# Kernel tuning notes

Measured on AMD Instinct MI355X. Metric: run time of the kernel, lower is better.

## Reference

```python
import jax, jax.numpy as jnp
import numpy as np

B, T, C, H = 4, 2048, 1024, 16
HD = C // H  # head_dim = 64

def setup_inputs() -> dict:
    key = jax.random.key(0)
    k1, k2, k3 = jax.random.split(key, 3)
    x = jax.random.normal(k1, (B, T, C), dtype=jnp.float32)
    w_qkv = jax.random.normal(k2, (C, 3 * C), dtype=jnp.float32) * (C ** -0.5)
    b_qkv = jnp.zeros((3 * C,), dtype=jnp.float32)
    w_proj = jax.random.normal(k3, (C, C), dtype=jnp.float32) * (C ** -0.5)
    b_proj = jnp.zeros((C,), dtype=jnp.float32)
    return {"x": x, "w_qkv": w_qkv, "b_qkv": b_qkv, "w_proj": w_proj, "b_proj": b_proj}

def reference(x, w_qkv, b_qkv, w_proj, b_proj):
    # QKV projection
    qkv = x @ w_qkv + b_qkv                      # [B,T,3C]
    q, k, v = jnp.split(qkv, 3, axis=-1)         # each [B,T,C]
    # split heads -> [B,H,T,HD]
    q = q.reshape(B, T, H, HD).transpose(0, 2, 1, 3)
    k = k.reshape(B, T, H, HD).transpose(0, 2, 1, 3)
    v = v.reshape(B, T, H, HD).transpose(0, 2, 1, 3)
    # muP attention: scale by 1/head_dim (not 1/sqrt)
    att = jnp.einsum('bhqd,bhkd->bhqk', q, k) * (1.0 / HD)  # [B,H,T,T]
    causal = jnp.tril(jnp.ones((T, T), dtype=bool))
    att = jnp.where(causal[None, None], att, -jnp.inf)
    att = jax.nn.softmax(att, axis=-1)
    # dropout = 0.0 (identity)
    y = jnp.einsum('bhqk,bhkd->bhqd', att, v)    # [B,H,T,HD]
    y = y.transpose(0, 2, 1, 3).reshape(B, T, C)
    y = y @ w_proj + b_proj
    return y
```

## Files before the change

### kernel.cpp

```cpp
#include <hip/hip_runtime.h>
#include <hip/hip_bf16.h>
#include <math.h>

typedef unsigned short ushort_t;
typedef unsigned int uint_t;
typedef __attribute__((ext_vector_type(8))) short short8;
typedef __attribute__((ext_vector_type(4))) float floatx4;
typedef __attribute__((ext_vector_type(2))) uint_t uint2v;

#define BB 4
#define TT 2048
#define CCH 1024
#define HH 16
#define HDIM 64
#define MROWS (BB * TT)

#define GLDS(g, l)                                                        \
  __builtin_amdgcn_global_load_lds(                                       \
      (const __attribute__((address_space(1))) void*)(g),                 \
      (__attribute__((address_space(3))) void*)(l), 16, 0, 0)

#if __has_builtin(__builtin_amdgcn_exp2f)
#define EXP2(x) __builtin_amdgcn_exp2f(x)
#else
#define EXP2(x) exp2f(x)
#endif

__device__ __forceinline__ ushort_t f2bf(float f) {
  union { float f; uint_t u; } x;
  x.f = f;
  uint_t u = x.u;
  u += 0x7FFFu + ((u >> 16) & 1u);
  return (ushort_t)(u >> 16);
}

__device__ __forceinline__ float bf2f(ushort_t v) {
  union { uint_t u; float f; } x;
  x.u = ((uint_t)v) << 16;
  return x.f;
}

__device__ __forceinline__ uint_t pk_trunc(float a, float b) {
  union { float f; uint_t u; } xa, xb;
  xa.f = a; xb.f = b;
  return (xa.u >> 16) | (xb.u & 0xFFFF0000u);
}

__device__ __forceinline__ uint_t pk_rne(float a, float b) {
  return (uint_t)f2bf(a) | ((uint_t)f2bf(b) << 16);
}

__global__ void detect_dtype(const uint_t* __restrict__ x, uint_t* __restrict__ flag) {
  __shared__ int cnt;
  if (threadIdx.x == 0) cnt = 0;
  __syncthreads();
  int c = 0;
  for (int i = threadIdx.x; i < 1024; i += 256) {
    uint_t w = x[i];
    uint_t e = (w >> 7) & 0xFFu;
    if (e >= 100u && e <= 150u) c++;
  }
  atomicAdd(&cnt, c);
  __syncthreads();
  if (threadIdx.x == 0) *flag = (cnt > 512) ? 1u : 0u;
}

__global__ void prep_x(const void* __restrict__ x, ushort_t* __restrict__ xb,
                       const uint_t* __restrict__ flag, int n) {
  int i = blockIdx.x * 256 + threadIdx.x;
  if (i >= n) return;
  if (*flag)
    xb[i] = ((const ushort_t*)x)[i];
  else
    xb[i] = f2bf(((const float*)x)[i]);
}

__global__ __launch_bounds__(256) void prep_wT(const void* __restrict__ w,
                                               ushort_t* __restrict__ wT,
                                               const uint_t* __restrict__ flag,
                                               int N) {
  __shared__ float tile[64][65];
  const int tid = threadIdx.x;
  const int bn = blockIdx.x * 64;
  const int bk = blockIdx.y * 64;
  if (*flag == 0) {
    const float* src = (const float*)w;
#pragma unroll
    for (int p = 0; p < 4; p++) {
      int r = p * 16 + (tid >> 4);
      int c = (tid & 15) * 4;
      float4 v = *(const float4*)&src[(size_t)(bk + r) * N + bn + c];
      tile[r][c] = v.x; tile[r][c + 1] = v.y;
      tile[r][c + 2] = v.z; tile[r][c + 3] = v.w;
    }
  } else {
    const ushort_t* src = (const ushort_t*)w;
#pragma unroll
    for (int p = 0; p < 4; p++) {
      int r = p * 16 + (tid >> 4);
      int c = (tid & 15) * 4;
      const ushort_t* s = &src[(size_t)(bk + r) * N + bn + c];
      tile[r][c] = bf2f(s[0]); tile[r][c + 1] = bf2f(s[1]);
      tile[r][c + 2] = bf2f(s[2]); tile[r][c + 3] = bf2f(s[3]);
    }
  }
  __syncthreads();
#pragma unroll
  for (int p = 0; p < 8; p++) {
    int nn = p * 8 + (tid >> 5);
    int kk = (tid & 31) * 2;
    uint_t u = pk_rne(tile[kk][nn], tile[kk + 1][nn]);
    *(uint_t*)&wT[(size_t)(bn + nn) * 1024 + bk + kk] = u;
  }
}

template <int MODE>
__global__ __launch_bounds__(256, 3) void gemm_bt(
    const ushort_t* __restrict__ A, const ushort_t* __restrict__ Bt,
    const void* __restrict__ bias,
    ushort_t* __restrict__ q_out, ushort_t* __restrict__ k_out,
    ushort_t* __restrict__ v_out, void* __restrict__ outp,
    const uint_t* __restrict__ flag) {
  alignas(16) __shared__ ushort_t As[3][128 * 32];
  alignas(16) __shared__ ushort_t Bs[3][128 * 32];

  const int tid = threadIdx.x;
  const int wave = tid >> 6, lane = tid & 63;
  const int quad = lane >> 4, l16 = lane & 15;
  const int wm = (wave & 1) * 64, wn = (wave >> 1) * 64;
  const int bm = blockIdx.x * 128, bn = blockIdx.y * 128;

  const int r0 = tid >> 2;
  const int co = ((tid & 3) ^ ((tid >> 3) & 3)) * 8;
  const int xs = (quad ^ ((l16 >> 1) & 3)) * 8;

  floatx4 acc[4][4] = {};

#define STAGE_G(kt, bf_)                                                     \
  do {                                                                       \
    const int k0_ = (kt) * 32;                                               \
    GLDS(&A[(size_t)(bm + r0) * 1024 + k0_ + co], &As[bf_][tid * 8]);        \
    GLDS(&A[(size_t)(bm + r0 + 64) * 1024 + k0_ + co],                       \
         &As[bf_][(tid + 256) * 8]);                                         \
    GLDS(&Bt[(size_t)(bn + r0) * 1024 + k0_ + co], &Bs[bf_][tid * 8]);       \
    GLDS(&Bt[(size_t)(bn + r0 + 64) * 1024 + k0_ + co],                      \
         &Bs[bf_][(tid + 256) * 8]);                                         \
  } while (0)

  STAGE_G(0, 0);
  STAGE_G(1, 1);
  STAGE_G(2, 2);

  int buf = 0;
  for (int kt = 0; kt < 32; kt++) {
    if (kt <= 29)
      asm volatile("s_waitcnt vmcnt(8)" ::: "memory");
    else if (kt == 30)
      asm volatile("s_waitcnt vmcnt(4)" ::: "memory");
    else
      asm volatile("s_waitcnt vmcnt(0)" ::: "memory");
    __builtin_amdgcn_s_barrier();
    __builtin_amdgcn_sched_barrier(0);

    short8 af[4], bf[4];
#pragma unroll
    for (int i = 0; i < 4; i++)
      af[i] = *(const short8*)&As[buf][(wm + i * 16 + l16) * 32 + xs];
#pragma unroll
    for (int i = 0; i < 4; i++)
      bf[i] = *(const short8*)&Bs[buf][(wn + i * 16 + l16) * 32 + xs];
    asm volatile("s_waitcnt lgkmcnt(0)" ::: "memory");
    __builtin_amdgcn_sched_barrier(0);
    __builtin_amdgcn_s_barrier();

    if (kt + 3 < 32) STAGE_G(kt + 3, buf);

    __builtin_amdgcn_s_setprio(1);
#pragma unroll
    for (int mi = 0; mi < 4; mi++)
#pragma unroll
      for (int ni = 0; ni < 4; ni++)
        acc[mi][ni] = __builtin_amdgcn_mfma_f32_16x16x32_bf16(
            af[mi], bf[ni], acc[mi][ni], 0, 0, 0);
    __builtin_amdgcn_s_setprio(0);

    buf = (buf == 2) ? 0 : buf + 1;
  }
#undef STAGE_G

  const bool inbf = (*flag != 0);

#pragma unroll
  for (int mi = 0; mi < 4; mi++) {
#pragma unroll
    for (int ni = 0; ni < 4; ni++) {
#pragma unroll
      for (int r = 0; r < 4; r++) {
        int row = bm + wm + mi * 16 + quad * 4 + r;
        int col = bn + wn + ni * 16 + l16;
        float bsv = inbf ? bf2f(((const ushort_t*)bias)[col])
                         : ((const float*)bias)[col];
        float v = acc[mi][ni][r] + bsv;
        if (MODE == 0) {
          ushort_t bv = f2bf(v);
          int b = row >> 11, t = row & 2047;
          int which = col >> 10, rem = col & 1023;
          int h = rem >> 6, d = rem & 63;
          size_t bh = (size_t)(b * HH + h);
          if (which == 0)
            q_out[(bh * TT + t) * HDIM + d] = bv;
          else if (which == 1)
            k_out[(bh * TT + t) * HDIM + d] = bv;
          else
            v_out[(bh * HDIM + d) * TT + t] = bv;
        } else {
          size_t idx = (size_t)row * CCH + col;
          if (inbf)
            ((ushort_t*)outp)[idx] = f2bf(v);
          else
            ((float*)outp)[idx] = v;
        }
      }
    }
  }
}

__global__ __launch_bounds__(256, 3) void flash_attn(
    const ushort_t* __restrict__ qb, const ushort_t* __restrict__ kb,
    const ushort_t* __restrict__ vtb, ushort_t* __restrict__ attb) {
  alignas(16) __shared__ ushort_t Ks[2][64 * 64];
  alignas(16) __shared__ ushort_t Vs[2][64 * 64];
  alignas(16) __shared__ ushort_t Ps[4][32 * 72];

  const int tid = threadIdx.x;
  const int wave = tid >> 6, lane = tid & 63;
  const int quad = lane >> 4, l16 = lane & 15;
  const int bh = blockIdx.x;
  const int b = bh >> 4, h = bh & 15;
  const int qt = 15 - blockIdx.y;
  const int qbs = qt * 128 + wave * 32;

  const ushort_t* Q = qb + (size_t)bh * TT * HDIM;
  const ushort_t* K = kb + (size_t)bh * TT * HDIM;
  const ushort_t* Vt = vtb + (size_t)bh * HDIM * TT;
  ushort_t* Pw = Ps[wave];

  const float SC = 0.015625f * 1.44269504089f;

  short8 qf[2][2];
#pragma unroll
  for (int m = 0; m < 2; m++)
#pragma unroll
    for (int ks = 0; ks < 2; ks++) {
      short8 a = *(const short8*)&Q[(size_t)(qbs + m * 16 + l16) * HDIM +
                                    ks * 32 + quad * 8];
#pragma unroll
      for (int j = 0; j < 8; j++)
        a[j] = (short)f2bf(bf2f((ushort_t)a[j]) * SC);
      qf[m][ks] = a;
    }

  short8 ones;
#pragma unroll
  for (int j = 0; j < 8; j++) ones[j] = (short)0x3F80;

  floatx4 o[2][4] = {};
  floatx4 osum[2] = {};

  const int lt = (qbs + 31) >> 6;
  const int ntiles = 2 * qt + 2;
  int cur = 0;

#pragma unroll
  for (int s2 = 0; s2 < 2; s2++) {
    int c = tid + s2 * 256;
    int row = c >> 3, gc = ((c & 7) ^ (row & 7)) * 8;
    GLDS(&K[(size_t)row * HDIM + gc], &Ks[0][c * 8]);
    GLDS(&Vt[(size_t)row * TT + gc], &Vs[0][c * 8]);
  }

  for (int kt = 0; kt < ntiles; kt++) {
    const int kt0 = kt * 64;
    cur = kt & 1;
    __syncthreads();

    if (kt + 1 < ntiles) {
      const int n0 = kt0 + 64;
#pragma unroll
      for (int s2 = 0; s2 < 2; s2++) {
        int c = tid + s2 * 256;
        int row = c >> 3, gc = ((c & 7) ^ (row & 7)) * 8;
        GLDS(&K[(size_t)(n0 + row) * HDIM + gc], &Ks[cur ^ 1][c * 8]);
        GLDS(&Vt[(size_t)row * TT + n0 + gc], &Vs[cur ^ 1][c * 8]);
      }
    }

    if (kt > lt) continue;

    short8 kf[4][2];
#pragma unroll
    for (int sub = 0; sub < 4; sub++)
#pragma unroll
      for (int ks = 0; ks < 2; ks++) {
        int col = (ks * 32 + quad * 8) ^ ((l16 & 7) * 8);
        kf[sub][ks] = *(const short8*)&Ks[cur][(sub * 16 + l16) * 64 + col];
      }

#pragma unroll
    for (int m = 0; m < 2; m++) {
      floatx4 s[4] = {};
      __builtin_amdgcn_s_setprio(1);
#pragma unroll
      for (int sub = 0; sub < 4; sub++)
#pragma unroll
        for (int ks = 0; ks < 2; ks++)
          s[sub] = __builtin_amdgcn_mfma_f32_16x16x32_bf16(
              kf[sub][ks], qf[m][ks], s[sub], 0, 0, 0);
      __builtin_amdgcn_s_setprio(0);

      const bool full = (kt0 + 63 <= qbs + m * 16);
      const int qrow = qbs + m * 16 + l16;
#pragma unroll
      for (int sub = 0; sub < 4; sub++) {
#pragma unroll
        for (int r = 0; r < 4; r++) {
          float p = EXP2(s[sub][r]);
          if (!full) {
            int key = kt0 + sub * 16 + quad * 4 + r;
            p = (key <= qrow) ? p : 0.0f;
          }
          s[sub][r] = p;
        }
        uint2v u;
        u[0] = pk_trunc(s[sub][0], s[sub][1]);
        u[1] = pk_trunc(s[sub][2], s[sub][3]);
        *(uint2v*)&Pw[(m * 16 + l16) * 72 + sub * 16 + quad * 4] = u;
      }
    }

    short8 pf[2][2];
#pragma unroll
    for (int m = 0; m < 2; m++)
#pragma unroll
      for (int ks = 0; ks < 2; ks++)
        pf[m][ks] =
            *(const short8*)&Pw[(m * 16 + l16) * 72 + ks * 32 + quad * 8];

    __builtin_amdgcn_s_setprio(1);
#pragma unroll
    for (int m = 0; m < 2; m++)
#pragma unroll
      for (int ks = 0; ks < 2; ks++)
        osum[m] = __builtin_amdgcn_mfma_f32_16x16x32_bf16(
            ones, pf[m][ks], osum[m], 0, 0, 0);

#pragma unroll
    for (int n = 0; n < 4; n++) {
#pragma unroll
      for (int ks = 0; ks < 2; ks++) {
        int col = (ks * 32 + quad * 8) ^ ((l16 & 7) * 8);
        short8 vf = *(const short8*)&Vs[cur][(n * 16 + l16) * 64 + col];
#pragma unroll
        for (int m = 0; m < 2; m++)
          o[m][n] = __builtin_amdgcn_mfma_f32_16x16x32_bf16(
              vf, pf[m][ks], o[m][n], 0, 0, 0);
      }
    }
    __builtin_amdgcn_s_setprio(0);
  }

#pragma unroll
  for (int m = 0; m < 2; m++) {
    float inv = 1.0f / osum[m][0];
    ushort_t* base =
        &attb[((size_t)(b * TT + qbs + m * 16 + l16)) * CCH + h * HDIM];
#pragma unroll
    for (int n = 0; n < 4; n++) {
      uint2v u;
      u[0] = pk_rne(o[m][n][0] * inv, o[m][n][1] * inv);
      u[1] = pk_rne(o[m][n][2] * inv, o[m][n][3] * inv);
      *(uint2v*)&base[n * 16 + quad * 4] = u;
    }
  }
}

extern "C" void kernel_launch(void* const* d_in, const int* in_sizes, int n_in,
                              void* d_out, int out_size, void* d_ws, size_t ws_size,
                              hipStream_t stream) {
  const void* x      = d_in[0];
  const void* w_qkv  = d_in[1];
  const void* b_qkv  = d_in[2];
  const void* w_proj = d_in[3];
  const void* b_proj = d_in[4];

  ushort_t* ws = (ushort_t*)d_ws;
  ushort_t* xb     = ws;
  ushort_t* wqkvT  = ws + 8388608;
  ushort_t* wprojT = ws + 11534336;
  ushort_t* qb     = ws + 12582912;
  ushort_t* kb     = ws + 20971520;
  ushort_t* attb   = xb;
  uint_t*   flag   = (uint_t*)(ws + 29360128);
  ushort_t* vtb    = (ushort_t*)d_out;

  detect_dtype<<<dim3(1), dim3(256), 0, stream>>>((const uint_t*)x, flag);

  prep_x<<<dim3((MROWS * CCH) / 256), dim3(256), 0, stream>>>(
      x, xb, flag, MROWS * CCH);
  prep_wT<<<dim3(48, 16), dim3(256), 0, stream>>>(w_qkv, wqkvT, flag, 3 * CCH);
  prep_wT<<<dim3(16, 16), dim3(256), 0, stream>>>(w_proj, wprojT, flag, CCH);

  gemm_bt<0><<<dim3(MROWS / 128, (3 * CCH) / 128), dim3(256), 0, stream>>>(
      xb, wqkvT, b_qkv, qb, kb, vtb, nullptr, flag);

  flash_attn<<<dim3(BB * HH, 16), dim3(256), 0, stream>>>(qb, kb, vtb, attb);

  gemm_bt<1><<<dim3(MROWS / 128, CCH / 128), dim3(256), 0, stream>>>(
      attb, wprojT, b_proj, nullptr, nullptr, nullptr, d_out, flag);
}
```

Before: 278.6 us.

## Double-buffer GEMM register fragments to overlap LDS reads with MFMA

Restructures the GEMM main loop so fragments for the next k-tile are read from LDS into a second register set while MFMAs run on the current set. The loop is unrolled by two so the A/B register buffers ping-pong, and one of the two barriers per iteration is dropped. This is meant to hide LDS read latency behind matrix math. The cost is doubled fragment registers, which may lower occupancy, and changed vmcnt wait counts that must stay correct for the three-stage global-to-LDS pipeline.

```diff
diff --git a/kernel.cpp b/kernel.cpp
--- a/kernel.cpp
+++ b/kernel.cpp
@@ -135,6 +135,7 @@
   const int xs = (quad ^ ((l16 >> 1) & 3)) * 8;
 
   floatx4 acc[4][4] = {};
+  short8 afA[4], bfA[4], afB[4], bfB[4];
 
 #define STAGE_G(kt, bf_)                                                     \
   do {                                                                       \
@@ -150,42 +151,49 @@
   STAGE_G(0, 0);
   STAGE_G(1, 1);
   STAGE_G(2, 2);
-
-  int buf = 0;
-  for (int kt = 0; kt < 32; kt++) {
-    if (kt <= 29)
-      asm volatile("s_waitcnt vmcnt(8)" ::: "memory");
-    else if (kt == 30)
-      asm volatile("s_waitcnt vmcnt(4)" ::: "memory");
-    else
-      asm volatile("s_waitcnt vmcnt(0)" ::: "memory");
-    __builtin_amdgcn_s_barrier();
-    __builtin_amdgcn_sched_barrier(0);
-
-    short8 af[4], bf[4];
-#pragma unroll
-    for (int i = 0; i < 4; i++)
-      af[i] = *(const short8*)&As[buf][(wm + i * 16 + l16) * 32 + xs];
-#pragma unroll
-    for (int i = 0; i < 4; i++)
-      bf[i] = *(const short8*)&Bs[buf][(wn + i * 16 + l16) * 32 + xs];
-    asm volatile("s_waitcnt lgkmcnt(0)" ::: "memory");
-    __builtin_amdgcn_sched_barrier(0);
-    __builtin_amdgcn_s_barrier();
-
-    if (kt + 3 < 32) STAGE_G(kt + 3, buf);
-
-    __builtin_amdgcn_s_setprio(1);
-#pragma unroll
-    for (int mi = 0; mi < 4; mi++)
-#pragma unroll
-      for (int ni = 0; ni < 4; ni++)
-        acc[mi][ni] = __builtin_amdgcn_mfma_f32_16x16x32_bf16(
-            af[mi], bf[ni], acc[mi][ni], 0, 0, 0);
-    __builtin_amdgcn_s_setprio(0);
-
-    buf = (buf == 2) ? 0 : buf + 1;
-  }
+  asm volatile("s_waitcnt vmcnt(8)" ::: "memory");
+  __builtin_amdgcn_s_barrier();
+  __builtin_amdgcn_sched_barrier(0);
+#pragma unroll
+  for (int i = 0; i < 4; i++)
+    afA[i] = *(const short8*)&As[0][(wm + i * 16 + l16) * 32 + xs];
+#pragma unroll
+  for (int i = 0; i < 4; i++)
+    bfA[i] = *(const short8*)&Bs[0][(wn + i * 16 + l16) * 32 + xs];
+  asm volatile("s_waitcnt lgkmcnt(0)" ::: "memory");
+  __builtin_amdgcn_sched_barrier(0);
+
+#define KBODY(kt, CA, CB, NA, NB)                                            \
+  {                                                                          \
+    if ((kt) <= 29)                                                          \
+      asm volatile("s_waitcnt vmcnt(4)" ::: "memory");                       \
+    else if ((kt) == 30)                                                     \
+      asm volatile("s_waitcnt vmcnt(0)" ::: "memory");                       \
+    __builtin_amdgcn_s_barrier();                                            \
+    __builtin_amdgcn_sched_barrier(0);                                       \
+    const int cs_ = (kt) % 3, ns_ = ((kt) + 1) % 3;                          \
+    if ((kt) + 3 < 32) STAGE_G((kt) + 3, cs_);                               \
+    if ((kt) + 1 < 32) {                                                     \
+      _Pragma("unroll") for (int i = 0; i < 4; i++)                          \
+          NA[i] = *(const short8*)&As[ns_][(wm + i * 16 + l16) * 32 + xs];   \
+      _Pragma("unroll") for (int i = 0; i < 4; i++)                          \
+          NB[i] = *(const short8*)&Bs[ns_][(wn + i * 16 + l16) * 32 + xs];   \
+    }                                                                        \
+    __builtin_amdgcn_s_setprio(1);                                           \
+    _Pragma("unroll") for (int mi = 0; mi < 4; mi++)                         \
+        _Pragma("unroll") for (int ni = 0; ni < 4; ni++)                     \
+            acc[mi][ni] = __builtin_amdgcn_mfma_f32_16x16x32_bf16(           \
+                CA[mi], CB[ni], acc[mi][ni], 0, 0, 0);                       \
+    __builtin_amdgcn_s_setprio(0);                                           \
+    asm volatile("s_waitcnt lgkmcnt(0)" ::: "memory");                       \
+    __builtin_amdgcn_sched_barrier(0);                                       \
+  }
+
+  for (int kt = 0; kt < 32; kt += 2) {
+    KBODY(kt, afA, bfA, afB, bfB);
+    KBODY(kt + 1, afB, bfB, afA, bfA);
+  }
+#undef KBODY
 #undef STAGE_G
 
   const bool inbf = (*flag != 0);
```

New measurement: 285.1 us. 1.02x slower.
